# Optimization experiments

Measured on AMD Instinct MI355X. Metric: run time of the kernel, lower is better.

## Reference

```python
import jax, jax.numpy as jnp
import numpy as np

N_HEADS = 8
TOPK = 64
LN_EPS = 1e-5


def layernorm(x, g, b):
    mu = jnp.mean(x, axis=-1, keepdims=True)
    var = jnp.mean((x - mu) ** 2, axis=-1, keepdims=True)
    return (x - mu) * jax.lax.rsqrt(var + LN_EPS) * g + b


def mha(x, wq, wk, wv, wo, causal):
    # x: [B, S, H]; weights are torch nn.Linear style [out, in]
    B, S, H = x.shape
    hd = H // N_HEADS
    scale = 1.0 / np.sqrt(hd)

    def proj(w):
        return (x @ w.T).reshape(B, S, N_HEADS, hd).transpose(0, 2, 1, 3)  # [B, n, S, hd]

    q, k, v = proj(wq), proj(wk), proj(wv)
    s = jnp.einsum('bnqd,bnkd->bnqk', q, k) * scale
    if causal:
        m = jnp.tril(jnp.ones((S, S), bool))
        s = jnp.where(m, s, jnp.finfo(s.dtype).min)
    a = jax.nn.softmax(s, axis=-1)
    o = jnp.einsum('bnqk,bnkd->bnqd', a, v).transpose(0, 2, 1, 3).reshape(B, S, H)
    return o @ wo.T


def topk_activation(x, k):
    # x: [N, F]; keep top-k per row, zero elsewhere (matches topk + scatter_)
    vals, idx = jax.lax.top_k(x, k)
    rows = jnp.arange(x.shape[0])[:, None]
    return jnp.zeros_like(x).at[rows, idx].set(vals)


def setup_inputs() -> dict:
    key = jax.random.key(0)
    B, D, L, H, F = 8, 16, 128, 512, 4096
    ks = jax.random.split(key, 12)
    s = 1.0 / np.sqrt(H)
    w = lambda k, shp, sc: jax.random.normal(k, shp, jnp.float32) * sc
    return {
        'zL': w(ks[0], (B, D, L, H), 1.0),
        'wq_l': w(ks[1], (H, H), s), 'wk_l': w(ks[2], (H, H), s),
        'wv_l': w(ks[3], (H, H), s), 'wo_l': w(ks[4], (H, H), s),
        'gamma_l': jnp.ones(H, jnp.float32), 'beta_l': jnp.zeros(H, jnp.float32),
        'wq_d': w(ks[5], (H, H), s), 'wk_d': w(ks[6], (H, H), s),
        'wv_d': w(ks[7], (H, H), s), 'wo_d': w(ks[8], (H, H), s),
        'gamma_d': jnp.ones(H, jnp.float32), 'beta_d': jnp.zeros(H, jnp.float32),
        'dict_enc': w(ks[9], (F, H), np.sqrt(2.0 / (H + F))),
        'bias_pre': jnp.zeros(H, jnp.float32),
        'bias_enc': jnp.zeros(F, jnp.float32),
        'query_token': jnp.zeros(H, jnp.float32),
    }


def reference(zL, wq_l, wk_l, wv_l, wo_l, gamma_l, beta_l,
              wq_d, wk_d, wv_d, wo_d, gamma_d, beta_d,
              dict_enc, bias_pre, bias_enc, query_token):
    B, D, L, H = zL.shape
    F = dict_enc.shape[0]
    # prepend learned query token along depth, drop last layer
    qt = jnp.broadcast_to(query_token[None, None, None, :], (B, 1, L, H))
    x = jnp.concatenate([qt, zL[:, :-1, :, :]], axis=1)  # [B, D, L, H]
    # non-causal attention over L within each (b, d)
    x = x.reshape(B * D, L, H)
    x = x + mha(layernorm(x, gamma_l, beta_l), wq_l, wk_l, wv_l, wo_l, causal=False)
    # causal attention over D within each (b, l)
    x = x.reshape(B, D, L, H).transpose(0, 2, 1, 3).reshape(B * L, D, H)
    x = x + mha(layernorm(x, gamma_d, beta_d), wq_d, wk_d, wv_d, wo_d, causal=True)
    x_prior = x.reshape(B, L, D, H).transpose(0, 2, 1, 3)  # [B, D, L, H]
    # dictionary encode on residual (detached in original)
    N = B * D * L
    x_src = jax.lax.stop_gradient(zL - x_prior).reshape(N, H)
    logits = (x_src - bias_pre[None, :]) @ dict_enc.T + bias_enc
    z_dense = jax.nn.relu(logits)
    z_flat = topk_activation(z_dense, TOPK)
    z_n = z_flat.reshape(B, D, L, F)
    return z_n, x_prior
```

## Files before the change

kernel.cpp:

```cpp
#include <hip/hip_runtime.h>
#include <stdint.h>

#define NTOK 16384
#define HDIM 512
#define FDIM 4096
#define NHEAD 8
#define QKVD 1536
#define L2E 1.44269504f

typedef __attribute__((ext_vector_type(8))) _Float16 f16x8;
typedef __attribute__((ext_vector_type(16))) float f32x16;
#define LOSCALE 4096.0f
#define LOINV   (1.0f / 4096.0f)

static __device__ __forceinline__ void ld8f(const float* p, float* v) {
    *(float4*)&v[0] = *(const float4*)p;
    *(float4*)&v[4] = *(const float4*)(p + 4);
}
static __device__ __forceinline__ void st8f(float* p, const float* v) {
    *(float4*)p       = *(const float4*)&v[0];
    *(float4*)(p + 4) = *(const float4*)&v[4];
}
static __device__ __forceinline__ uint32_t packsplit(float v) {
    _Float16 h = (_Float16)v;
    _Float16 l = (_Float16)((v - (float)h) * LOSCALE);
    union { _Float16 f; uint16_t u; } ch{h}, cl{l};
    return (uint32_t)ch.u | ((uint32_t)cl.u << 16);
}
static __device__ __forceinline__ void unpack8(const uint32_t* p, f16x8* h, f16x8* l) {
    union { uint16_t s[8]; f16x8 v; } uh, ul;
#pragma unroll
    for (int i = 0; i < 8; ++i) {
        uint32_t x = p[i];
        uh.s[i] = (uint16_t)(x & 0xffffu);
        ul.s[i] = (uint16_t)(x >> 16);
    }
    *h = uh.v;
    *l = ul.v;
}

__global__ __launch_bounds__(256) void build_x_k(const float* __restrict__ zL,
                                                 const float* __restrict__ qt,
                                                 float* __restrict__ X) {
    int idx = blockIdx.x * 256 + threadIdx.x;
    int n = idx >> 6;
    int h = (idx & 63) << 3;
    int d = (n >> 7) & 15;
    const float* src = d ? (zL + (((size_t)(n - 128)) << 9) + h) : (qt + h);
    float v[8];
    ld8f(src, v);
    st8f(X + (((size_t)n) << 9) + h, v);
}

__global__ __launch_bounds__(256) void ln_split_k(const float* __restrict__ X,
                                                  const float* __restrict__ gamma,
                                                  const float* __restrict__ beta,
                                                  _Float16* __restrict__ ph,
                                                  _Float16* __restrict__ pl) {
    int row = blockIdx.x * 4 + (threadIdx.x >> 6);
    int lane = threadIdx.x & 63;
    int h = lane << 3;
    const float* xr = X + (((size_t)row) << 9) + h;
    float v[8];
    ld8f(xr, v);
    float s = 0.f;
#pragma unroll
    for (int i = 0; i < 8; ++i) s += v[i];
#pragma unroll
    for (int off = 32; off; off >>= 1) s += __shfl_xor(s, off);
    float m = s * (1.0f / 512.0f);
    float q = 0.f;
#pragma unroll
    for (int i = 0; i < 8; ++i) { float d = v[i] - m; q += d * d; }
#pragma unroll
    for (int off = 32; off; off >>= 1) q += __shfl_xor(q, off);
    float rs = 1.0f / sqrtf(q * (1.0f / 512.0f) + 1e-5f);
    float gv[8], be[8];
    ld8f(gamma + h, gv);
    ld8f(beta + h, be);
    _Float16 h8[8], l8[8];
#pragma unroll
    for (int i = 0; i < 8; ++i) {
        float y = (v[i] - m) * rs * gv[i] + be[i];
        _Float16 hh = (_Float16)y;
        h8[i] = hh;
        l8[i] = (_Float16)((y - (float)hh) * LOSCALE);
    }
    size_t off = (((size_t)row) << 9) + h;
    *(int4*)(ph + off) = *(int4*)h8;
    *(int4*)(pl + off) = *(int4*)l8;
}

__global__ __launch_bounds__(256) void attn_l_k(const float* __restrict__ QKV,
                                                _Float16* __restrict__ xh,
                                                _Float16* __restrict__ xl) {
    __shared__ uint32_t pool[25024];
    uint32_t* Qp = pool;
    uint32_t* Kp = pool + 8320;
    uint32_t* Vt = pool + 16640;
    float*    rl = (float*)(pool + 24896);
    uint32_t* S  = pool;

    const int seq = blockIdx.x, head = blockIdx.y;
    const int t = threadIdx.x;
    const size_t tok0 = (size_t)seq << 7;
    const int ho = head << 6;
    const int w = t >> 6, lane = t & 63;
    const int wr = w >> 1, wc = w & 1;
    const int l31 = lane & 31, hh = lane >> 5;

#pragma unroll
    for (int i = 0; i < 8; ++i) {
        int idx = t + (i << 8);
        int row = idx >> 4, c4 = (idx & 15) << 2;
        size_t g = (tok0 + row) * QKVD + ho + c4;
        float4 qv = *(const float4*)(QKV + g);
        float4 kv = *(const float4*)(QKV + g + 512);
        float4 vv = *(const float4*)(QKV + g + 1024);
        uint32_t* qd = Qp + row * 65 + c4;
        qd[0] = packsplit(qv.x); qd[1] = packsplit(qv.y);
        qd[2] = packsplit(qv.z); qd[3] = packsplit(qv.w);
        uint32_t* kd = Kp + row * 65 + c4;
        kd[0] = packsplit(kv.x); kd[1] = packsplit(kv.y);
        kd[2] = packsplit(kv.z); kd[3] = packsplit(kv.w);
        Vt[(c4 + 0) * 129 + row] = packsplit(vv.x);
        Vt[(c4 + 1) * 129 + row] = packsplit(vv.y);
        Vt[(c4 + 2) * 129 + row] = packsplit(vv.z);
        Vt[(c4 + 3) * 129 + row] = packsplit(vv.w);
    }
    __syncthreads();

    f32x16 a1[2][2], a2[2][2];
#pragma unroll
    for (int i = 0; i < 2; ++i)
#pragma unroll
        for (int j = 0; j < 2; ++j)
#pragma unroll
            for (int r = 0; r < 16; ++r) { a1[i][j][r] = 0.f; a2[i][j][r] = 0.f; }
#pragma unroll
    for (int ks = 0; ks < 4; ++ks) {
        const int ko = (ks << 4) + (hh << 3);
        f16x8 qh[2], ql[2], kh[2], kl[2];
#pragma unroll
        for (int mf = 0; mf < 2; ++mf)
            unpack8(Qp + ((wr << 6) + (mf << 5) + l31) * 65 + ko, &qh[mf], &ql[mf]);
#pragma unroll
        for (int nf = 0; nf < 2; ++nf)
            unpack8(Kp + ((wc << 6) + (nf << 5) + l31) * 65 + ko, &kh[nf], &kl[nf]);
#pragma unroll
        for (int nf = 0; nf < 2; ++nf)
#pragma unroll
            for (int mf = 0; mf < 2; ++mf) {
                a1[mf][nf] = __builtin_amdgcn_mfma_f32_32x32x16_f16(qh[mf], kh[nf], a1[mf][nf], 0, 0, 0);
                a2[mf][nf] = __builtin_amdgcn_mfma_f32_32x32x16_f16(qh[mf], kl[nf], a2[mf][nf], 0, 0, 0);
                a2[mf][nf] = __builtin_amdgcn_mfma_f32_32x32x16_f16(ql[mf], kh[nf], a2[mf][nf], 0, 0, 0);
            }
    }
    __syncthreads();
#pragma unroll
    for (int mf = 0; mf < 2; ++mf)
#pragma unroll
        for (int nf = 0; nf < 2; ++nf) {
            int col = (wc << 6) + (nf << 5) + l31;
#pragma unroll
            for (int r = 0; r < 16; ++r) {
                int row = (wr << 6) + (mf << 5) + (r & 3) + ((r >> 2) << 3) + (hh << 2);
                float sv = (a1[mf][nf][r] + a2[mf][nf][r] * LOINV) * 0.125f;
                S[row * 129 + col] = __float_as_uint(sv);
            }
        }
    __syncthreads();

    {
        int row = t >> 1, half = t & 1;
        uint32_t* sr = S + row * 129 + (half << 6);
        float mx = -1e30f;
#pragma unroll
        for (int j = 0; j < 64; ++j) mx = fmaxf(mx, __uint_as_float(sr[j]));
        mx = fmaxf(mx, __shfl_xor(mx, 1));
        float sum = 0.f;
#pragma unroll
        for (int j = 0; j < 64; ++j) {
            float wg = exp2f((__uint_as_float(sr[j]) - mx) * L2E);
            sum += wg;
            sr[j] = packsplit(wg);
        }
        sum += __shfl_xor(sum, 1);
        if (!half) rl[row] = 1.0f / sum;
    }
    __syncthreads();

    f32x16 o1[2], o2[2];
#pragma unroll
    for (int i = 0; i < 2; ++i)
#pragma unroll
        for (int r = 0; r < 16; ++r) { o1[i][r] = 0.f; o2[i][r] = 0.f; }
    const int dcol = (wc << 5) + l31;
#pragma unroll
    for (int ks = 0; ks < 8; ++ks) {
        const int jo = (ks << 4) + (hh << 3);
        f16x8 ph[2], pl2[2], vh, vl;
#pragma unroll
        for (int mf = 0; mf < 2; ++mf)
            unpack8(S + ((wr << 6) + (mf << 5) + l31) * 129 + jo, &ph[mf], &pl2[mf]);
        unpack8(Vt + dcol * 129 + jo, &vh, &vl);
#pragma unroll
        for (int mf = 0; mf < 2; ++mf) {
            o1[mf] = __builtin_amdgcn_mfma_f32_32x32x16_f16(ph[mf], vh, o1[mf], 0, 0, 0);
            o2[mf] = __builtin_amdgcn_mfma_f32_32x32x16_f16(ph[mf], vl, o2[mf], 0, 0, 0);
            o2[mf] = __builtin_amdgcn_mfma_f32_32x32x16_f16(pl2[mf], vh, o2[mf], 0, 0, 0);
        }
    }
#pragma unroll
    for (int mf = 0; mf < 2; ++mf)
#pragma unroll
        for (int r = 0; r < 16; ++r) {
            int row = (wr << 6) + (mf << 5) + (r & 3) + ((r >> 2) << 3) + (hh << 2);
            float y = (o1[mf][r] + o2[mf][r] * LOINV) * rl[row];
            size_t eo = ((tok0 + row) << 9) + ho + dcol;
            _Float16 hv = (_Float16)y;
            xh[eo] = hv;
            xl[eo] = (_Float16)((y - (float)hv) * LOSCALE);
        }
}

__global__ __launch_bounds__(128) void attn_d_k(const float* __restrict__ QKV,
                                                _Float16* __restrict__ xh,
                                                _Float16* __restrict__ xl) {
    __shared__ float ks[16][512];
    __shared__ float vs[16][512];
    const int bl = blockIdx.x;
    const int b = bl >> 7, l = bl & 127;
    const int t = threadIdx.x;
    const size_t tok0 = (size_t)b * 2048 + l;
#pragma unroll
    for (int i = 0; i < 16; ++i) {
        int c4 = t << 2;
        int hc = c4 >> 6;
        int p  = (c4 & ~63) | ((c4 + (hc << 2)) & 63);
        size_t g = (tok0 + (size_t)i * 128) * QKVD + c4;
        *(float4*)&ks[i][p] = *(const float4*)(QKV + g + 512);
        *(float4*)&vs[i][p] = *(const float4*)(QKV + g + 1024);
    }
    __syncthreads();
    const int head = t >> 4, dr = t & 15;
    const int ho = head << 6;
    const int rot = head << 2;
    float qr[64];
    const float* qp = QKV + (tok0 + (size_t)dr * 128) * QKVD + ho;
#pragma unroll
    for (int i = 0; i < 16; ++i) *(float4*)&qr[i << 2] = *(const float4*)(qp + (i << 2));
    float s[16];
    float m = -1e30f;
#pragma unroll
    for (int j = 0; j < 16; ++j) {
        float s0 = 0.f, s1 = 0.f, s2 = 0.f, s3 = 0.f;
#pragma unroll
        for (int d = 0; d < 64; d += 4) {
            s0 = fmaf(qr[d + 0], ks[j][ho + ((d + 0 + rot) & 63)], s0);
            s1 = fmaf(qr[d + 1], ks[j][ho + ((d + 1 + rot) & 63)], s1);
            s2 = fmaf(qr[d + 2], ks[j][ho + ((d + 2 + rot) & 63)], s2);
            s3 = fmaf(qr[d + 3], ks[j][ho + ((d + 3 + rot) & 63)], s3);
        }
        float sv = ((s0 + s1) + (s2 + s3)) * 0.125f;
        s[j] = (j <= dr) ? sv : -1e30f;
        m = fmaxf(m, s[j]);
    }
    float lsum = 0.f;
#pragma unroll
    for (int j = 0; j < 16; ++j) {
        float w = (j <= dr) ? exp2f((s[j] - m) * L2E) : 0.f;
        s[j] = w;
        lsum += w;
    }
    float inv = 1.0f / lsum;
    float o[64];
#pragma unroll
    for (int d = 0; d < 64; ++d) o[d] = 0.f;
#pragma unroll
    for (int j = 0; j < 16; ++j) {
        float w = s[j];
#pragma unroll
        for (int d = 0; d < 64; ++d) o[d] = fmaf(w, vs[j][ho + ((d + rot) & 63)], o[d]);
    }
    size_t eo = ((tok0 + (size_t)dr * 128) << 9) + ho;
#pragma unroll
    for (int i = 0; i < 8; ++i) {
        _Float16 h8[8], l8[8];
#pragma unroll
        for (int j = 0; j < 8; ++j) {
            float y = o[i * 8 + j] * inv;
            _Float16 hh = (_Float16)y;
            h8[j] = hh;
            l8[j] = (_Float16)((y - (float)hh) * LOSCALE);
        }
        *(int4*)(xh + eo + (i << 3)) = *(int4*)h8;
        *(int4*)(xl + eo + (i << 3)) = *(int4*)l8;
    }
}

__global__ __launch_bounds__(256) void xprior_xsrc_k(const float* __restrict__ zL,
                                                     const float* __restrict__ bias_pre,
                                                     const float* __restrict__ X,
                                                     float* __restrict__ out_xp,
                                                     _Float16* __restrict__ xh,
                                                     _Float16* __restrict__ xl) {
    int idx = blockIdx.x * 256 + threadIdx.x;
    int h = (idx & 63) << 3;
    size_t off = ((size_t)idx) << 3;
    float z[8], p[8], x[8];
    ld8f(zL + off, z);
    ld8f(bias_pre + h, p);
    ld8f(X + off, x);
    st8f(out_xp + off, x);
    _Float16 h8[8], l8[8];
#pragma unroll
    for (int i = 0; i < 8; ++i) {
        float y = z[i] - x[i] - p[i];
        _Float16 hh = (_Float16)y;
        h8[i] = hh;
        l8[i] = (_Float16)((y - (float)hh) * LOSCALE);
    }
    *(int4*)(xh + off) = *(int4*)h8;
    *(int4*)(xl + off) = *(int4*)l8;
}

__global__ __launch_bounds__(256) void split2_k(const float* __restrict__ in,
                                                _Float16* __restrict__ ph,
                                                _Float16* __restrict__ pl) {
    int idx = blockIdx.x * 256 + threadIdx.x;
    float v[8];
    ld8f(in + (((size_t)idx) << 3), v);
    _Float16 h8[8], l8[8];
#pragma unroll
    for (int i = 0; i < 8; ++i) {
        _Float16 h = (_Float16)v[i];
        float r = v[i] - (float)h;
        h8[i] = h;
        l8[i] = (_Float16)(r * LOSCALE);
    }
    *(int4*)(ph + (((size_t)idx) << 3)) = *(int4*)h8;
    *(int4*)(pl + (((size_t)idx) << 3)) = *(int4*)l8;
}

#define LDT 34
template<int SWZ, bool ADD_C, bool BIAS>
__global__ __launch_bounds__(256) void gemm_f16_k(
        const _Float16* __restrict__ Xh, const _Float16* __restrict__ Xl,
        const _Float16* __restrict__ Wh, const _Float16* __restrict__ Wl,
        const float* __restrict__ bias, float* __restrict__ Cout, int ldc) {
    __shared__ _Float16 Ah[2][128][LDT], Al[2][128][LDT];
    __shared__ _Float16 Bh[2][64][LDT],  Bl[2][64][LDT];
    const int tid = threadIdx.x;
    int bm, bn;
    if (SWZ) {
        int id = blockIdx.x;
        int xcd = id & 7, ww = id >> 3;
        bn = ((xcd << 3) | (ww & 7)) << 6;
        bm = (ww >> 3) << 7;
    } else {
        bm = blockIdx.y << 7;
        bn = blockIdx.x << 6;
    }
    const int w = tid >> 6, lane = tid & 63;
    const int wr = w >> 1, wc = w & 1;
    const int l31 = lane & 31, hh = lane >> 5;
    const int ar0 = tid >> 2, akg = (tid & 3) << 3;
    const int ar1 = ar0 + 64;
    const _Float16* pXh0 = Xh + (size_t)(bm + ar0) * HDIM + akg;
    const _Float16* pXl0 = Xl + (size_t)(bm + ar0) * HDIM + akg;
    const _Float16* pXh1 = Xh + (size_t)(bm + ar1) * HDIM + akg;
    const _Float16* pXl1 = Xl + (size_t)(bm + ar1) * HDIM + akg;
    const _Float16* pWh  = Wh + (size_t)(bn + ar0) * HDIM + akg;
    const _Float16* pWl  = Wl + (size_t)(bn + ar0) * HDIM + akg;

    f32x16 acc1[2], acc2[2];
#pragma unroll
    for (int i = 0; i < 2; ++i)
#pragma unroll
        for (int r = 0; r < 16; ++r) { acc1[i][r] = 0.f; acc2[i][r] = 0.f; }

    int4 ra0h, ra0l, ra1h, ra1l, rbh, rbl;
    auto LOADR = [&](int k0) {
        ra0h = *(const int4*)(pXh0 + k0);
        ra0l = *(const int4*)(pXl0 + k0);
        ra1h = *(const int4*)(pXh1 + k0);
        ra1l = *(const int4*)(pXl1 + k0);
        rbh  = *(const int4*)(pWh + k0);
        rbl  = *(const int4*)(pWl + k0);
    };
    auto STORE = [&](int buf) {
        *(int4*)&Ah[buf][ar0][akg] = ra0h;
        *(int4*)&Al[buf][ar0][akg] = ra0l;
        *(int4*)&Ah[buf][ar1][akg] = ra1h;
        *(int4*)&Al[buf][ar1][akg] = ra1l;
        *(int4*)&Bh[buf][ar0][akg] = rbh;
        *(int4*)&Bl[buf][ar0][akg] = rbl;
    };

    LOADR(0);
    STORE(0);
    int cur = 0;
    for (int it = 0; it < 16; ++it) {
        if (it < 15) LOADR((it + 1) << 5);
        __syncthreads();
#pragma unroll
        for (int kh = 0; kh < 2; ++kh) {
            const int ko = (kh << 4) + (hh << 3);
            f16x8 fah[2], fal[2];
#pragma unroll
            for (int mf = 0; mf < 2; ++mf) {
                int ar = (wr << 6) + (mf << 5) + l31;
                fah[mf] = *(const f16x8*)&Ah[cur][ar][ko];
                fal[mf] = *(const f16x8*)&Al[cur][ar][ko];
            }
            int bc_ = (wc << 5) + l31;
            f16x8 bh = *(const f16x8*)&Bh[cur][bc_][ko];
            f16x8 bl = *(const f16x8*)&Bl[cur][bc_][ko];
#pragma unroll
            for (int mf = 0; mf < 2; ++mf) {
                acc1[mf] = __builtin_amdgcn_mfma_f32_32x32x16_f16(fah[mf], bh, acc1[mf], 0, 0, 0);
                acc2[mf] = __builtin_amdgcn_mfma_f32_32x32x16_f16(fah[mf], bl, acc2[mf], 0, 0, 0);
                acc2[mf] = __builtin_amdgcn_mfma_f32_32x32x16_f16(fal[mf], bh, acc2[mf], 0, 0, 0);
            }
        }
        if (it < 15) { STORE(cur ^ 1); cur ^= 1; }
    }
    const int col = bn + (wc << 5) + l31;
    const float badd = BIAS ? bias[col] : 0.f;
#pragma unroll
    for (int mf = 0; mf < 2; ++mf) {
#pragma unroll
        for (int r = 0; r < 16; ++r) {
            int row = bm + (wr << 6) + (mf << 5) + (r & 3) + ((r >> 2) << 3) + (hh << 2);
            float* cp = Cout + (size_t)row * ldc + col;
            float val = acc1[mf][r] + acc2[mf][r] * LOINV + badd;
            if (ADD_C) val += *cp;
            *cp = val;
        }
    }
}

__global__ __launch_bounds__(256) void topk_k(const float* __restrict__ logits,
                                              float* __restrict__ out) {
    const int row = blockIdx.x;
    const float* lr = logits + (((size_t)row) << 12);
    const int t = threadIdx.x;
    float v[16]; uint32_t u[16];
#pragma unroll
    for (int i = 0; i < 16; ++i) {
        float x = fmaxf(lr[t + (i << 8)], 0.f);
        v[i] = x;
        u[i] = __float_as_uint(x);
    }
    __shared__ int red[4];
    __shared__ unsigned long long bits[64];
    __shared__ int s_cut;
    uint32_t prefix = 0;
    bool exact = false;
    for (int bit = 30; bit >= 0; --bit) {
        uint32_t c = prefix | (1u << bit);
        int cnt = 0;
#pragma unroll
        for (int i = 0; i < 16; ++i) cnt += (u[i] >= c) ? 1 : 0;
#pragma unroll
        for (int off = 32; off; off >>= 1) cnt += __shfl_xor(cnt, off);
        if ((t & 63) == 0) red[t >> 6] = cnt;
        __syncthreads();
        int total = red[0] + red[1] + red[2] + red[3];
        __syncthreads();
        if (total >= 64) prefix = c;
        if (total == 64) { exact = true; break; }
    }
    float* orow = out + (((size_t)row) << 12);
    if (exact) {
#pragma unroll
        for (int i = 0; i < 16; ++i) {
            int col = t + (i << 8);
            orow[col] = (u[i] >= prefix) ? v[i] : 0.f;
        }
        return;
    }
    const uint32_t T64 = prefix;
    int cg = 0;
#pragma unroll
    for (int i = 0; i < 16; ++i) cg += (u[i] > T64) ? 1 : 0;
#pragma unroll
    for (int off = 32; off; off >>= 1) cg += __shfl_xor(cg, off);
    if ((t & 63) == 0) red[t >> 6] = cg;
    __syncthreads();
    const int ngt = red[0] + red[1] + red[2] + red[3];
    int cut = -1;
    if (T64 != 0u) {
        const int r = 64 - ngt;
        if (t < 64) bits[t] = 0ull;
        __syncthreads();
#pragma unroll
        for (int i = 0; i < 16; ++i) {
            if (u[i] == T64) {
                int col = t + (i << 8);
                atomicOr(&bits[col >> 6], 1ull << (col & 63));
            }
        }
        __syncthreads();
        if (t == 0) {
            int need = r, cs = FDIM - 1;
            for (int wd = 0; wd < 64; ++wd) {
                int pc = __popcll(bits[wd]);
                if (need <= pc) {
                    unsigned long long bb = bits[wd];
                    for (int q = 1; q < need; ++q) bb &= bb - 1;
                    cs = (wd << 6) + (__ffsll(bb) - 1);
                    break;
                }
                need -= pc;
            }
            s_cut = cs;
        }
        __syncthreads();
        cut = s_cut;
    }
#pragma unroll
    for (int i = 0; i < 16; ++i) {
        int col = t + (i << 8);
        bool keep = (u[i] > T64) || (T64 != 0u && u[i] == T64 && col <= cut);
        orow[col] = keep ? v[i] : 0.f;
    }
}

extern "C" void kernel_launch(void* const* d_in, const int* in_sizes, int n_in,
                              void* d_out, int out_size, void* d_ws, size_t ws_size,
                              hipStream_t stream) {
    const float* zL      = (const float*)d_in[0];
    const float* gamma_l = (const float*)d_in[5];
    const float* beta_l  = (const float*)d_in[6];
    const float* gamma_d = (const float*)d_in[11];
    const float* beta_d  = (const float*)d_in[12];
    const float* dict_e  = (const float*)d_in[13];
    const float* bias_pre= (const float*)d_in[14];
    const float* bias_enc= (const float*)d_in[15];
    const float* qt      = (const float*)d_in[16];
    const float* wproj[8] = { (const float*)d_in[1], (const float*)d_in[2],
                              (const float*)d_in[3], (const float*)d_in[4],
                              (const float*)d_in[7], (const float*)d_in[8],
                              (const float*)d_in[9], (const float*)d_in[10] };

    float* out_z  = (float*)d_out;
    float* out_xp = out_z + (size_t)NTOK * FDIM;

    const size_t NHf = (size_t)NTOK * HDIM;
    float* B0 = (float*)d_out;
    float* B1 = B0 + NHf;

    float* wsf    = (float*)d_ws;
    float* logits = wsf + 64;

    const size_t dictE = (size_t)FDIM * HDIM;
    const size_t WE    = (size_t)HDIM * HDIM;

    int crows = 2048;
    const size_t fixedB = 64 * sizeof(float)
                        + (2 * dictE + 16 * WE + 2 * NHf) * sizeof(_Float16);
    while (crows > 128 && fixedB + (size_t)crows * FDIM * sizeof(float) > ws_size)
        crows >>= 1;

    _Float16* dh  = (_Float16*)(logits + (size_t)crows * FDIM);
    _Float16* dl  = dh + dictE;
    _Float16* wsp = dh + 2 * dictE;
    _Float16* xh  = wsp + 16 * WE;
    _Float16* xl  = xh + NHf;
    _Float16* qkvh_l = wsp;
    _Float16* qkvl_l = wsp + 3 * WE;
    _Float16* woh_l  = wsp + 6 * WE;
    _Float16* wol_l  = wsp + 7 * WE;
    _Float16* qkvh_d = wsp + 8 * WE;
    _Float16* qkvl_d = wsp + 11 * WE;
    _Float16* woh_d  = wsp + 14 * WE;
    _Float16* wol_d  = wsp + 15 * WE;

    const dim3 blk256(256), blk128(128);
    const dim3 gElem(4096);
    const dim3 gW(WE / 8 / 256);
    const dim3 gQKV(QKVD / 64, NTOK / 128);
    const dim3 gWo(HDIM / 64, NTOK / 128);

    split2_k<<<gW, blk256, 0, stream>>>(wproj[0], qkvh_l,          qkvl_l);
    split2_k<<<gW, blk256, 0, stream>>>(wproj[1], qkvh_l + WE,     qkvl_l + WE);
    split2_k<<<gW, blk256, 0, stream>>>(wproj[2], qkvh_l + 2 * WE, qkvl_l + 2 * WE);
    split2_k<<<gW, blk256, 0, stream>>>(wproj[3], woh_l,           wol_l);
    split2_k<<<gW, blk256, 0, stream>>>(wproj[4], qkvh_d,          qkvl_d);
    split2_k<<<gW, blk256, 0, stream>>>(wproj[5], qkvh_d + WE,     qkvl_d + WE);
    split2_k<<<gW, blk256, 0, stream>>>(wproj[6], qkvh_d + 2 * WE, qkvl_d + 2 * WE);
    split2_k<<<gW, blk256, 0, stream>>>(wproj[7], woh_d,           wol_d);
    split2_k<<<dim3(dictE / 8 / 256), blk256, 0, stream>>>(dict_e, dh, dl);

    build_x_k<<<gElem, blk256, 0, stream>>>(zL, qt, B0);

    ln_split_k<<<dim3(NTOK / 4), blk256, 0, stream>>>(B0, gamma_l, beta_l, xh, xl);
    gemm_f16_k<0, false, false><<<gQKV, blk256, 0, stream>>>(xh, xl, qkvh_l, qkvl_l, nullptr, B1, QKVD);
    attn_l_k<<<dim3(128, NHEAD), blk256, 0, stream>>>(B1, xh, xl);
    gemm_f16_k<0, true, false><<<gWo, blk256, 0, stream>>>(xh, xl, woh_l, wol_l, nullptr, B0, HDIM);

    ln_split_k<<<dim3(NTOK / 4), blk256, 0, stream>>>(B0, gamma_d, beta_d, xh, xl);
    gemm_f16_k<0, false, false><<<gQKV, blk256, 0, stream>>>(xh, xl, qkvh_d, qkvl_d, nullptr, B1, QKVD);
    attn_d_k<<<dim3(1024), blk128, 0, stream>>>(B1, xh, xl);
    gemm_f16_k<0, true, false><<<gWo, blk256, 0, stream>>>(xh, xl, woh_d, wol_d, nullptr, B0, HDIM);

    xprior_xsrc_k<<<gElem, blk256, 0, stream>>>(zL, bias_pre, B0, out_xp, xh, xl);

    for (int c0 = 0; c0 < NTOK; c0 += crows) {
        if ((crows & 127) == 0 && (crows / 128) * 64 % 8 == 0) {
            gemm_f16_k<1, false, true><<<dim3(64 * (crows / 128)), blk256, 0, stream>>>(
                xh + (size_t)c0 * HDIM, xl + (size_t)c0 * HDIM,
                dh, dl, bias_enc, logits, FDIM);
        } else {
            gemm_f16_k<0, false, true><<<dim3(FDIM / 64, crows / 128), blk256, 0, stream>>>(
                xh + (size_t)c0 * HDIM, xl + (size_t)c0 * HDIM,
                dh, dl, bias_enc, logits, FDIM);
        }
        topk_k<<<dim3(crows), blk256, 0, stream>>>(logits, out_z + (size_t)c0 * FDIM);
    }
}
```

Measured before the change: 1.067 ms.

## Batch weight splits into one launch, double-buffer topk reduction, enlarge logits chunk

The eight per-weight fp16 hi/lo split launches become a single kernel that picks its source weight by block index, with the workspace relaid so the high and low halves of all weights are each contiguous. The topk radix-select loop now alternates between two reduction slots, which removes one block barrier per bit iteration. The logits chunk size doubles to 4096 rows when the workspace allows it, which halves the number of chunked encode/topk launches. These cut launch overhead and barrier cost, and the larger chunk needs more workspace.

```diff
diff --git a/kernel.cpp b/kernel.cpp
--- a/kernel.cpp
+++ b/kernel.cpp
@@ -341,6 +341,37 @@
     }
     *(int4*)(ph + (((size_t)idx) << 3)) = *(int4*)h8;
     *(int4*)(pl + (((size_t)idx) << 3)) = *(int4*)l8;
+}
+
+__global__ __launch_bounds__(256) void split2w_k(const float* __restrict__ w0,
+                                                 const float* __restrict__ w1,
+                                                 const float* __restrict__ w2,
+                                                 const float* __restrict__ w3,
+                                                 const float* __restrict__ w4,
+                                                 const float* __restrict__ w5,
+                                                 const float* __restrict__ w6,
+                                                 const float* __restrict__ w7,
+                                                 _Float16* __restrict__ dsth,
+                                                 _Float16* __restrict__ dstl,
+                                                 int perW, int WEsz) {
+    int wsel = blockIdx.x / perW;
+    int bid  = blockIdx.x % perW;
+    const float* src = wsel == 0 ? w0 : wsel == 1 ? w1 : wsel == 2 ? w2 : wsel == 3 ? w3
+                    : wsel == 4 ? w4 : wsel == 5 ? w5 : wsel == 6 ? w6 : w7;
+    int idx = bid * 256 + threadIdx.x;
+    float v[8];
+    ld8f(src + (((size_t)idx) << 3), v);
+    _Float16 h8[8], l8[8];
+#pragma unroll
+    for (int i = 0; i < 8; ++i) {
+        _Float16 h = (_Float16)v[i];
+        float r = v[i] - (float)h;
+        h8[i] = h;
+        l8[i] = (_Float16)(r * LOSCALE);
+    }
+    size_t off = (size_t)wsel * WEsz + (((size_t)idx) << 3);
+    *(int4*)(dsth + off) = *(int4*)h8;
+    *(int4*)(dstl + off) = *(int4*)l8;
 }
 
 #define LDT 34
@@ -453,22 +484,22 @@
         v[i] = x;
         u[i] = __float_as_uint(x);
     }
-    __shared__ int red[4];
+    __shared__ int red[2][4];
     __shared__ unsigned long long bits[64];
     __shared__ int s_cut;
     uint32_t prefix = 0;
     bool exact = false;
-    for (int bit = 30; bit >= 0; --bit) {
+    int par = 0;
+    for (int bit = 30; bit >= 0; --bit, par ^= 1) {
         uint32_t c = prefix | (1u << bit);
         int cnt = 0;
 #pragma unroll
         for (int i = 0; i < 16; ++i) cnt += (u[i] >= c) ? 1 : 0;
 #pragma unroll
         for (int off = 32; off; off >>= 1) cnt += __shfl_xor(cnt, off);
-        if ((t & 63) == 0) red[t >> 6] = cnt;
+        if ((t & 63) == 0) red[par][t >> 6] = cnt;
         __syncthreads();
-        int total = red[0] + red[1] + red[2] + red[3];
-        __syncthreads();
+        int total = red[par][0] + red[par][1] + red[par][2] + red[par][3];
         if (total >= 64) prefix = c;
         if (total == 64) { exact = true; break; }
     }
@@ -487,9 +518,10 @@
     for (int i = 0; i < 16; ++i) cg += (u[i] > T64) ? 1 : 0;
 #pragma unroll
     for (int off = 32; off; off >>= 1) cg += __shfl_xor(cg, off);
-    if ((t & 63) == 0) red[t >> 6] = cg;
     __syncthreads();
-    const int ngt = red[0] + red[1] + red[2] + red[3];
+    if ((t & 63) == 0) red[0][t >> 6] = cg;
+    __syncthreads();
+    const int ngt = red[0][0] + red[0][1] + red[0][2] + red[0][3];
     int cut = -1;
     if (T64 != 0u) {
         const int r = 64 - ngt;
@@ -540,10 +572,10 @@
     const float* bias_pre= (const float*)d_in[14];
     const float* bias_enc= (const float*)d_in[15];
     const float* qt      = (const float*)d_in[16];
-    const float* wproj[8] = { (const float*)d_in[1], (const float*)d_in[2],
-                              (const float*)d_in[3], (const float*)d_in[4],
-                              (const float*)d_in[7], (const float*)d_in[8],
-                              (const float*)d_in[9], (const float*)d_in[10] };
+    const float* worder[8] = { (const float*)d_in[1], (const float*)d_in[2],
+                               (const float*)d_in[3], (const float*)d_in[4],
+                               (const float*)d_in[7], (const float*)d_in[8],
+                               (const float*)d_in[9], (const float*)d_in[10] };
 
     float* out_z  = (float*)d_out;
     float* out_xp = out_z + (size_t)NTOK * FDIM;
@@ -558,7 +590,7 @@
     const size_t dictE = (size_t)FDIM * HDIM;
     const size_t WE    = (size_t)HDIM * HDIM;
 
-    int crows = 2048;
+    int crows = 4096;
     const size_t fixedB = 64 * sizeof(float)
                         + (2 * dictE + 16 * WE + 2 * NHf) * sizeof(_Float16);
     while (crows > 128 && fixedB + (size_t)crows * FDIM * sizeof(float) > ws_size)
@@ -566,32 +598,29 @@
 
     _Float16* dh  = (_Float16*)(logits + (size_t)crows * FDIM);
     _Float16* dl  = dh + dictE;
-    _Float16* wsp = dh + 2 * dictE;
-    _Float16* xh  = wsp + 16 * WE;
+    _Float16* wsph = dh + 2 * dictE;
+    _Float16* wspl = wsph + 8 * WE;
+    _Float16* xh  = wspl + 8 * WE;
     _Float16* xl  = xh + NHf;
-    _Float16* qkvh_l = wsp;
-    _Float16* qkvl_l = wsp + 3 * WE;
-    _Float16* woh_l  = wsp + 6 * WE;
-    _Float16* wol_l  = wsp + 7 * WE;
-    _Float16* qkvh_d = wsp + 8 * WE;
-    _Float16* qkvl_d = wsp + 11 * WE;
-    _Float16* woh_d  = wsp + 14 * WE;
-    _Float16* wol_d  = wsp + 15 * WE;
+    _Float16* qkvh_l = wsph;
+    _Float16* qkvl_l = wspl;
+    _Float16* woh_l  = wsph + 3 * WE;
+    _Float16* wol_l  = wspl + 3 * WE;
+    _Float16* qkvh_d = wsph + 4 * WE;
+    _Float16* qkvl_d = wspl + 4 * WE;
+    _Float16* woh_d  = wsph + 7 * WE;
+    _Float16* wol_d  = wspl + 7 * WE;
 
     const dim3 blk256(256), blk128(128);
     const dim3 gElem(4096);
-    const dim3 gW(WE / 8 / 256);
+    const int perW = (int)(WE / 8 / 256);
     const dim3 gQKV(QKVD / 64, NTOK / 128);
     const dim3 gWo(HDIM / 64, NTOK / 128);
 
-    split2_k<<<gW, blk256, 0, stream>>>(wproj[0], qkvh_l,          qkvl_l);
-    split2_k<<<gW, blk256, 0, stream>>>(wproj[1], qkvh_l + WE,     qkvl_l + WE);
-    split2_k<<<gW, blk256, 0, stream>>>(wproj[2], qkvh_l + 2 * WE, qkvl_l + 2 * WE);
-    split2_k<<<gW, blk256, 0, stream>>>(wproj[3], woh_l,           wol_l);
-    split2_k<<<gW, blk256, 0, stream>>>(wproj[4], qkvh_d,          qkvl_d);
-    split2_k<<<gW, blk256, 0, stream>>>(wproj[5], qkvh_d + WE,     qkvl_d + WE);
-    split2_k<<<gW, blk256, 0, stream>>>(wproj[6], qkvh_d + 2 * WE, qkvl_d + 2 * WE);
-    split2_k<<<gW, blk256, 0, stream>>>(wproj[7], woh_d,           wol_d);
+    split2w_k<<<dim3(8 * perW), blk256, 0, stream>>>(
+        worder[0], worder[1], worder[2], worder[3],
+        worder[4], worder[5], worder[6], worder[7],
+        wsph, wspl, perW, (int)WE);
     split2_k<<<dim3(dictE / 8 / 256), blk256, 0, stream>>>(dict_e, dh, dl);
 
     build_x_k<<<gElem, blk256, 0, stream>>>(zL, qt, B0);
```

Result: faster. 991.4 us (-7.1%).
